# Kernel tuning notes

Hardware: AMD Instinct MI355X
Metric: run time of the kernel (lower is better)

The kernel has to match this reference:

```python
import jax, jax.numpy as jnp
from jax import lax
import numpy as np

DN = ('NCHW', 'OIHW', 'NCHW')
EPS = 1e-5


def conv3(x, w, b=None):
    # 3x3 conv, stride 1, padding 1 (SAME)
    y = lax.conv_general_dilated(x, w, (1, 1), 'SAME', dimension_numbers=DN)
    return y if b is None else y + b[None, :, None, None]


def bn_relu(x, gamma, beta):
    # training-mode BatchNorm2d (batch statistics over N,H,W) + ReLU
    m = jnp.mean(x, axis=(0, 2, 3), keepdims=True)
    v = jnp.var(x, axis=(0, 2, 3), keepdims=True)
    y = (x - m) * lax.rsqrt(v + EPS)
    y = y * gamma[None, :, None, None] + beta[None, :, None, None]
    return jax.nn.relu(y)


def _w(key, o, i):
    # torch init: normal(0, sqrt(2/(k*k*out)))
    std = np.sqrt(2.0 / (3 * 3 * o))
    return jax.random.normal(key, (o, i, 3, 3), dtype=jnp.float32) * std


def setup_inputs() -> dict:
    key = jax.random.key(0)
    ks = jax.random.split(key, 16)
    C = 256
    Ch = C // 2
    B, H, W = 4, 160, 160
    d = {}
    d['fpn_fea'] = jax.random.normal(ks[0], (B, C, H, W), dtype=jnp.float32)
    # sc_smooth_layer: conv(C->C)+BN+ReLU, conv(C->C/2)+BN+ReLU (no conv bias)
    d['w_sc1'] = _w(ks[1], C, C); d['g_sc1'] = jnp.ones((C,)); d['b_sc1'] = jnp.zeros((C,))
    d['w_sc2'] = _w(ks[2], Ch, C); d['g_sc2'] = jnp.ones((Ch,)); d['b_sc2'] = jnp.zeros((Ch,))
    # shrink / centroid heads: plain conv(C/2 -> 1) with bias
    d['w_shrink'] = _w(ks[3], 1, Ch); d['bias_shrink'] = jnp.zeros((1,))
    d['w_cent'] = _w(ks[4], 1, Ch); d['bias_cent'] = jnp.zeros((1,))
    # param_head
    d['w_p1'] = _w(ks[5], C, C); d['g_p1'] = jnp.ones((C,)); d['b_p1'] = jnp.zeros((C,))
    d['w_p2'] = _w(ks[6], Ch, C); d['g_p2'] = jnp.ones((Ch,)); d['b_p2'] = jnp.zeros((Ch,))
    d['w_p3'] = _w(ks[7], 2, Ch); d['bias_p3'] = jnp.zeros((2,))
    # shift_head
    d['w_s1'] = _w(ks[8], C, C); d['g_s1'] = jnp.ones((C,)); d['b_s1'] = jnp.zeros((C,))
    d['w_s2'] = _w(ks[9], Ch, C); d['g_s2'] = jnp.ones((Ch,)); d['b_s2'] = jnp.zeros((Ch,))
    d['w_s3'] = _w(ks[10], 8, Ch); d['bias_s3'] = jnp.zeros((8,))
    return d


def reference(fpn_fea, w_sc1, g_sc1, b_sc1, w_sc2, g_sc2, b_sc2,
              w_shrink, bias_shrink, w_cent, bias_cent,
              w_p1, g_p1, b_p1, w_p2, g_p2, b_p2, w_p3, bias_p3,
              w_s1, g_s1, b_s1, w_s2, g_s2, b_s2, w_s3, bias_s3):
    smooth = bn_relu(conv3(fpn_fea, w_sc1), g_sc1, b_sc1)
    smooth = bn_relu(conv3(smooth, w_sc2), g_sc2, b_sc2)
    shrink = conv3(smooth, w_shrink, bias_shrink)      # [B,1,H,W]
    centroid = conv3(smooth, w_cent, bias_cent)        # [B,1,H,W]
    p = bn_relu(conv3(fpn_fea, w_p1), g_p1, b_p1)
    p = bn_relu(conv3(p, w_p2), g_p2, b_p2)
    param = conv3(p, w_p3, bias_p3)                    # [B,2,H,W]
    s = bn_relu(conv3(fpn_fea, w_s1), g_s1, b_s1)
    s = bn_relu(conv3(s, w_s2), g_s2, b_s2)
    shift = conv3(s, w_s3, bias_s3)                    # [B,8,H,W]
    return (shrink, centroid, param, shift)
```

## Files before the change

### kernel.cpp

```cpp
#include <hip/hip_runtime.h>

typedef short bf16x8 __attribute__((ext_vector_type(8)));
typedef float f32x4 __attribute__((ext_vector_type(4)));

__device__ __forceinline__ float bf2f(unsigned short u) {
    union { unsigned int i; float f; } c; c.i = ((unsigned int)u) << 16; return c.f;
}
__device__ __forceinline__ unsigned short f2bf(float f) {
    union { float f; unsigned int i; } c; c.f = f;
    unsigned int u = c.i;
    u += 0x7fffu + ((u >> 16) & 1u);
    return (unsigned short)(u >> 16);
}

__device__ __forceinline__ void gload_lds16(const unsigned short* g, unsigned short* l) {
    __builtin_amdgcn_global_load_lds(
        (const __attribute__((address_space(1))) void*)g,
        (__attribute__((address_space(3))) void*)l, 16, 0, 0);
}

__global__ void transpose_pad(const float* __restrict__ x, unsigned short* __restrict__ xpad) {
    int idx = blockIdx.x * 256 + threadIdx.x;
    int w = idx % 160; int t = idx / 160;
    int cv = t % 32;   t /= 32;
    int h = t % 160;   int n = t / 160;
    const float* src = x + (((size_t)(n * 256 + cv * 8) * 160 + h) * 160 + w);
    unsigned short us[8];
#pragma unroll
    for (int k = 0; k < 8; ++k) us[k] = f2bf(src[(size_t)k * 25600]);
    uint4 o;
    o.x = (unsigned int)us[0] | ((unsigned int)us[1] << 16);
    o.y = (unsigned int)us[2] | ((unsigned int)us[3] << 16);
    o.z = (unsigned int)us[4] | ((unsigned int)us[5] << 16);
    o.w = (unsigned int)us[6] | ((unsigned int)us[7] << 16);
    *(uint4*)(xpad + ((size_t)((n * 162 + h + 1) * 162) + (w + 1)) * 256 + cv * 8) = o;
}

__device__ __forceinline__ void zero_border_one(unsigned short* buf, int C, int idx) {
    int CV = C >> 3;
    int cv = idx % CV; int t = idx / CV;
    int p = t % 644;   int n = t / 644;
    int h, w;
    if (p < 162)      { h = 0;   w = p; }
    else if (p < 324) { h = 161; w = p - 162; }
    else { int q = p - 324; h = 1 + (q >> 1); w = (q & 1) ? 161 : 0; }
    uint4 z = make_uint4(0u, 0u, 0u, 0u);
    *(uint4*)(buf + ((size_t)((n * 162 + h) * 162) + w) * C + cv * 8) = z;
}

__global__ void zero_all(unsigned short* __restrict__ xpad,
                         unsigned short* __restrict__ buf1, size_t s1,
                         unsigned short* __restrict__ buf2, size_t s2, int nbr) {
    int idx = blockIdx.x * 256 + threadIdx.x;
    if (idx < 82432) { zero_border_one(xpad, 256, idx); return; }
    idx -= 82432;
    int nb1 = nbr * 82432;
    if (idx < nb1) { zero_border_one(buf1 + (size_t)(idx / 82432) * s1, 256, idx % 82432); return; }
    idx -= nb1;
    int nb2 = nbr * 41216;
    if (idx < nb2) { zero_border_one(buf2 + (size_t)(idx / 41216) * s2, 128, idx % 41216); }
}

__global__ void pack_all(const float* __restrict__ s0, const float* __restrict__ s1,
                         const float* __restrict__ s2, const float* __restrict__ s3,
                         const float* __restrict__ s4, const float* __restrict__ s5,
                         unsigned short* __restrict__ w1p, unsigned short* __restrict__ w2p) {
    int idx = blockIdx.x * 256 + threadIdx.x;
    int t = idx / 294912, r = idx - t * 294912;
    const float* src; unsigned short* dst; int coBase;
    if (t < 6) {
        int br = t >> 1;
        src = (br == 0) ? s0 : (br == 1) ? s1 : s2;
        coBase = (t & 1) * 128;
        dst = w1p + (size_t)t * 294912;
    } else {
        int br = t - 6;
        src = (br == 0) ? s3 : (br == 1) ? s4 : s5;
        coBase = 0;
        dst = w2p + (size_t)br * 294912;
    }
    int tap, ci, o;
    if (r < 262144) {
        int tp = r >> 16, rem = r & 65535;
        int q = rem >> 13, r2 = rem & 8191;
        int e = r2 & 7, gco = r2 >> 3;
        int co = gco & 127, g = gco >> 7;
        tap = tp * 2 + (g >> 2);
        ci = q * 32 + (g & 3) * 8 + e;
        o = coBase + co;
    } else {
        int rem = r - 262144;
        int q = rem >> 12, r2 = rem & 4095;
        int e = r2 & 7, gco = r2 >> 3;
        int co = gco & 127, g = gco >> 7;
        tap = 8;
        ci = q * 32 + g * 8 + e;
        o = coBase + co;
    }
    dst[r] = f2bf(src[((size_t)(o * 256 + ci)) * 9 + tap]);
}

template<int COT, int BPB>
__global__ __launch_bounds__(256, 2) void conv3x3_mfma(
        const unsigned short* __restrict__ xpad0, size_t xstride,
        const unsigned short* __restrict__ wpk0, size_t wstride,
        unsigned short* __restrict__ ypad0, size_t ystride,
        float* __restrict__ stats, int sstride) {
    __shared__ __align__(16) unsigned short As[16384];
    __shared__ __align__(16) unsigned short Bs[12288];

    const int br = blockIdx.x / BPB;
    int bid = blockIdx.x % BPB;
    const unsigned short* xpad = xpad0 + (size_t)br * xstride;
    const unsigned short* wpk  = wpk0 + (size_t)br * wstride;
    unsigned short* ypad       = ypad0 + (size_t)br * ystride;
    float* sum   = stats + (size_t)br * sstride;
    float* sumsq = sum + 256;

    const int tid = threadIdx.x;
    const int wv = tid >> 6, lane = tid & 63;
    const int quad = lane >> 4, l15 = lane & 15;
    const int wco = wv >> 1, wsp = wv & 1;

    const int wt = bid % 5;
    const int ht = (bid / 5) % 20;
    const int n = (bid / 100) % 4;
    const int tile = bid / 400;
    const int co0 = tile * 128;
    const int h0 = ht * 8, w0 = wt * 32;

    const unsigned short* wtile = wpk + (size_t)tile * 294912;

    int boff[6];
#pragma unroll
    for (int r = 0; r < 6; ++r) {
        int slot = r * 256 + tid;
        int g = slot / 384, p = slot - g * 384;
        if (p > 339) p = 339;
        int prow = p / 34, pcol = p - prow * 34;
        boff[r] = ((n * 162 + h0 + prow) * 162 + (w0 + pcol)) * 256 + g * 8;
    }

    int p0[8];
#pragma unroll
    for (int j = 0; j < 8; ++j) {
        int sp = wsp * 128 + j * 16 + l15;
        p0[j] = (sp >> 5) * 34 + (sp & 31);
    }

    f32x4 acc[4][8];
#pragma unroll
    for (int i = 0; i < 4; ++i)
#pragma unroll
        for (int j = 0; j < 8; ++j) acc[i][j] = (f32x4){0.f, 0.f, 0.f, 0.f};

    for (int q = 0; q < 8; ++q) {
#pragma unroll
        for (int w = 0; w < 3; ++w) {
            __syncthreads();
            if (w == 0) {
                const unsigned short* bq = xpad + q * 32;
#pragma unroll
                for (int r = 0; r < 6; ++r)
                    gload_lds16(bq + boff[r], (unsigned short*)Bs + (r * 256 + tid) * 8);
            }
            if (w < 2) {
#pragma unroll
                for (int h = 0; h < 2; ++h) {
                    const unsigned short* asrc = wtile + (w * 2 + h) * 65536 + q * 8192 + tid * 8;
#pragma unroll
                    for (int c = 0; c < 4; ++c)
                        gload_lds16(asrc + c * 2048,
                                    (unsigned short*)As + h * 8192 + c * 2048 + tid * 8);
                }
            } else {
                const unsigned short* asrc = wtile + 262144 + q * 4096 + tid * 8;
#pragma unroll
                for (int c = 0; c < 2; ++c)
                    gload_lds16(asrc + c * 2048, (unsigned short*)As + c * 2048 + tid * 8);
            }
            __syncthreads();

#pragma unroll
            for (int t = 0; t < 4; ++t) {
                if (w == 2 && t >= 1) continue;
                const int TAP = (w < 2) ? (w * 4 + t) : 8;
                const int dh = TAP / 3, dw = TAP % 3;
                const int toff = dh * 34 + dw;
                const int g0 = (w < 2) ? ((t & 1) * 4 + quad) : quad;
                const unsigned short* Ab = As + ((w < 2) ? (t >> 1) * 8192 : 0);
                bf16x8 a[4];
#pragma unroll
                for (int i = 0; i < 4; ++i)
                    a[i] = *(const bf16x8*)(Ab + (size_t)(g0 * 128 + wco * 64 + i * 16 + l15) * 8);
#pragma unroll
                for (int jh = 0; jh < 2; ++jh) {
                    bf16x8 b[4];
#pragma unroll
                    for (int j = 0; j < 4; ++j)
                        b[j] = *(const bf16x8*)(Bs + (size_t)(quad * 384 + p0[jh * 4 + j] + toff) * 8);
#pragma unroll
                    for (int i = 0; i < 4; ++i)
#pragma unroll
                        for (int j = 0; j < 4; ++j)
                            acc[i][jh * 4 + j] = __builtin_amdgcn_mfma_f32_16x16x32_bf16(
                                a[i], b[j], acc[i][jh * 4 + j], 0, 0, 0);
                }
            }
        }
    }

#pragma unroll
    for (int i = 0; i < 4; ++i) {
        const int co_l = wco * 64 + i * 16 + quad * 4;
#pragma unroll
        for (int j = 0; j < 8; ++j) {
            const int sp = wsp * 128 + j * 16 + l15;
            const int jh = sp >> 5, jw = sp & 31;
            f32x4 v = acc[i][j];
            ushort4 pk;
            pk.x = f2bf(v[0]); pk.y = f2bf(v[1]); pk.z = f2bf(v[2]); pk.w = f2bf(v[3]);
            *(ushort4*)(ypad + ((size_t)((n * 162 + h0 + jh + 1) * 162) + (w0 + jw + 1)) * COT
                        + co0 + co_l) = pk;
        }
#pragma unroll
        for (int r = 0; r < 4; ++r) {
            float s1 = 0.f, s2 = 0.f;
#pragma unroll
            for (int j = 0; j < 8; ++j) { float v = acc[i][j][r]; s1 += v; s2 += v * v; }
#pragma unroll
            for (int m = 1; m < 16; m <<= 1) {
                s1 += __shfl_xor(s1, m, 64);
                s2 += __shfl_xor(s2, m, 64);
            }
            if (l15 == 0) {
                atomicAdd(&sum[co0 + co_l + r], s1);
                atomicAdd(&sumsq[co0 + co_l + r], s2);
            }
        }
    }
}

template<int C, int BPB>
__global__ void bn_apply(unsigned short* __restrict__ buf0, size_t bstride,
                         const float* __restrict__ stats, int sstride,
                         const float* g0, const float* g1, const float* g2,
                         const float* be0, const float* be1, const float* be2) {
    const int br = blockIdx.x / BPB;
    unsigned short* buf = buf0 + (size_t)br * bstride;
    const float* sum = stats + (size_t)br * sstride;
    const float* sumsq = sum + 256;
    const float* gamma = (br == 0) ? g0 : (br == 1) ? g1 : g2;
    const float* beta  = (br == 0) ? be0 : (br == 1) ? be1 : be2;

    __shared__ float s_sc[C], s_sh[C];
    if (threadIdx.x < C) {
        int c = threadIdx.x;
        const float inv = 1.0f / 102400.0f;
        float m = sum[c] * inv;
        float v = sumsq[c] * inv - m * m;
        float sc = gamma[c] * rsqrtf(v + 1e-5f);
        s_sc[c] = sc;
        s_sh[c] = beta[c] - m * sc;
    }
    __syncthreads();

    constexpr int CV = C / 8;
    int idx = (blockIdx.x % BPB) * 256 + threadIdx.x;
    int cv = idx % CV; int pos = idx / CV;
    int w = pos % 160; int h = (pos / 160) % 160; int n = pos / 25600;
    unsigned short* p = buf + ((size_t)((n * 162 + h + 1) * 162) + (w + 1)) * C + cv * 8;
    uint4 v = *(const uint4*)p;
    unsigned int ua[4] = {v.x, v.y, v.z, v.w};
    unsigned int ob[4];
#pragma unroll
    for (int j = 0; j < 4; ++j) {
        int c = cv * 8 + j * 2;
        float f0 = bf2f((unsigned short)(ua[j] & 0xffffu)) * s_sc[c] + s_sh[c];
        float f1 = bf2f((unsigned short)(ua[j] >> 16)) * s_sc[c + 1] + s_sh[c + 1];
        f0 = fmaxf(f0, 0.f); f1 = fmaxf(f1, 0.f);
        ob[j] = (unsigned int)f2bf(f0) | ((unsigned int)f2bf(f1) << 16);
    }
    uint4 o = make_uint4(ob[0], ob[1], ob[2], ob[3]);
    *(uint4*)p = o;
}

template<int CO>
__global__ __launch_bounds__(256) void head_conv(const unsigned short* __restrict__ z,
                                                 const float* __restrict__ w,
                                                 const float* __restrict__ bias,
                                                 float* __restrict__ out) {
    __shared__ float s_w[CO * 9 * 128];
    for (int t = threadIdx.x; t < CO * 9 * 128; t += 256) {
        int ci = t % 128; int r = t / 128;
        int tap = r % 9;  int o = r / 9;
        s_w[t] = w[((size_t)(o * 128 + ci)) * 9 + tap];
    }
    __syncthreads();

    const int pos = blockIdx.x * 256 + threadIdx.x;
    const int pw = pos % 160, ph = (pos / 160) % 160, pn = pos / 25600;
    float acc[CO];
#pragma unroll
    for (int o = 0; o < CO; ++o) acc[o] = bias[o];

#pragma unroll
    for (int dh = 0; dh < 3; ++dh)
#pragma unroll
        for (int dw = 0; dw < 3; ++dw) {
            const int tap = dh * 3 + dw;
            const unsigned short* zp = z + ((size_t)((pn * 162 + ph + dh) * 162) + (pw + dw)) * 128;
            for (int c8 = 0; c8 < 16; ++c8) {
                uint4 v = *(const uint4*)(zp + c8 * 8);
                unsigned int ua[4] = {v.x, v.y, v.z, v.w};
                float xv[8];
#pragma unroll
                for (int j = 0; j < 4; ++j) {
                    xv[2 * j]     = bf2f((unsigned short)(ua[j] & 0xffffu));
                    xv[2 * j + 1] = bf2f((unsigned short)(ua[j] >> 16));
                }
#pragma unroll
                for (int o = 0; o < CO; ++o) {
                    const float* wp = &s_w[(o * 9 + tap) * 128 + c8 * 8];
                    float4 w0 = *(const float4*)wp;
                    float4 w1 = *(const float4*)(wp + 4);
                    acc[o] = fmaf(xv[0], w0.x, acc[o]);
                    acc[o] = fmaf(xv[1], w0.y, acc[o]);
                    acc[o] = fmaf(xv[2], w0.z, acc[o]);
                    acc[o] = fmaf(xv[3], w0.w, acc[o]);
                    acc[o] = fmaf(xv[4], w1.x, acc[o]);
                    acc[o] = fmaf(xv[5], w1.y, acc[o]);
                    acc[o] = fmaf(xv[6], w1.z, acc[o]);
                    acc[o] = fmaf(xv[7], w1.w, acc[o]);
                }
            }
        }
#pragma unroll
    for (int o = 0; o < CO; ++o)
        out[((size_t)(pn * CO + o)) * 25600 + ph * 160 + pw] = acc[o];
}

__global__ __launch_bounds__(256) void head_conv_dual(const unsigned short* __restrict__ z,
                                                      const float* __restrict__ w1, const float* __restrict__ b1,
                                                      const float* __restrict__ w2, const float* __restrict__ b2,
                                                      float* __restrict__ out1, float* __restrict__ out2) {
    __shared__ float s_w[2 * 9 * 128];
    for (int t = threadIdx.x; t < 2 * 9 * 128; t += 256) {
        int ci = t % 128; int r = t / 128;
        int tap = r % 9;  int which = r / 9;
        const float* src = which ? w2 : w1;
        s_w[t] = src[(size_t)ci * 9 + tap];
    }
    __syncthreads();

    const int pos = blockIdx.x * 256 + threadIdx.x;
    const int pw = pos % 160, ph = (pos / 160) % 160, pn = pos / 25600;
    float a1 = b1[0], a2 = b2[0];

#pragma unroll
    for (int dh = 0; dh < 3; ++dh)
#pragma unroll
        for (int dw = 0; dw < 3; ++dw) {
            const int tap = dh * 3 + dw;
            const unsigned short* zp = z + ((size_t)((pn * 162 + ph + dh) * 162) + (pw + dw)) * 128;
            for (int c8 = 0; c8 < 16; ++c8) {
                uint4 v = *(const uint4*)(zp + c8 * 8);
                unsigned int ua[4] = {v.x, v.y, v.z, v.w};
                float xv[8];
#pragma unroll
                for (int j = 0; j < 4; ++j) {
                    xv[2 * j]     = bf2f((unsigned short)(ua[j] & 0xffffu));
                    xv[2 * j + 1] = bf2f((unsigned short)(ua[j] >> 16));
                }
                const float* wp1 = &s_w[tap * 128 + c8 * 8];
                const float* wp2 = &s_w[1152 + tap * 128 + c8 * 8];
#pragma unroll
                for (int e = 0; e < 8; ++e) {
                    a1 = fmaf(xv[e], wp1[e], a1);
                    a2 = fmaf(xv[e], wp2[e], a2);
                }
            }
        }
    out1[(size_t)pn * 25600 + ph * 160 + pw] = a1;
    out2[(size_t)pn * 25600 + ph * 160 + pw] = a2;
}

extern "C" void kernel_launch(void* const* d_in, const int* in_sizes, int n_in,
                              void* d_out, int out_size, void* d_ws, size_t ws_size,
                              hipStream_t stream) {
    const float* fpn = (const float*)d_in[0];
    const float* W1[3] = {(const float*)d_in[1],  (const float*)d_in[11], (const float*)d_in[19]};
    const float* G1[3] = {(const float*)d_in[2],  (const float*)d_in[12], (const float*)d_in[20]};
    const float* B1[3] = {(const float*)d_in[3],  (const float*)d_in[13], (const float*)d_in[21]};
    const float* W2[3] = {(const float*)d_in[4],  (const float*)d_in[14], (const float*)d_in[22]};
    const float* G2[3] = {(const float*)d_in[5],  (const float*)d_in[15], (const float*)d_in[23]};
    const float* B2[3] = {(const float*)d_in[6],  (const float*)d_in[16], (const float*)d_in[24]};
    const float* w_shrink = (const float*)d_in[7];  const float* b_shrink = (const float*)d_in[8];
    const float* w_cent   = (const float*)d_in[9];  const float* b_cent   = (const float*)d_in[10];
    const float* w_p3     = (const float*)d_in[17]; const float* b_p3     = (const float*)d_in[18];
    const float* w_s3     = (const float*)d_in[25]; const float* b_s3     = (const float*)d_in[26];
    float* out = (float*)d_out;

    const size_t S1 = (size_t)4 * 162 * 162 * 256;
    const size_t S2 = (size_t)4 * 162 * 162 * 128;
    const size_t need_fused = S1 * 2 * 4  + S2 * 2 * 3
                              + (size_t)9 * 294912 * 2 + 6 * 512 * 4;

    char* ws = (char*)d_ws;
    size_t off = 0;
    unsigned short* xpad = (unsigned short*)(ws + off); off += S1 * 2;
    const int NBR = (ws_size >= need_fused) ? 3 : 1;
    unsigned short* buf1 = (unsigned short*)(ws + off); off += S1 * 2 * NBR;
    unsigned short* buf2 = (unsigned short*)(ws + off); off += S2 * 2 * NBR;
    unsigned short* w1p  = (unsigned short*)(ws + off); off += (size_t)6 * 294912 * 2;
    unsigned short* w2p  = (unsigned short*)(ws + off); off += (size_t)3 * 294912 * 2;
    float* stats         = (float*)(ws + off);          off += (size_t)6 * 512 * 4;

    hipMemsetAsync(stats, 0, 6 * 512 * 4, stream);
    {
        int zthreads = 82432 * (1 + NBR) + 41216 * NBR;
        zero_all<<<(zthreads + 255) / 256, 256, 0, stream>>>(xpad, buf1, S1, buf2, S2, NBR);
    }
    transpose_pad<<<12800, 256, 0, stream>>>(fpn, xpad);
    pack_all<<<10368, 256, 0, stream>>>(W1[0], W1[1], W1[2], W2[0], W2[1], W2[2], w1p, w2p);

    if (NBR == 3) {
        conv3x3_mfma<256, 800><<<2400, 256, 0, stream>>>(
            xpad, 0, w1p, (size_t)2 * 294912, buf1, S1, stats, 1024);
        bn_apply<256, 12800><<<38400, 256, 0, stream>>>(
            buf1, S1, stats, 1024, G1[0], G1[1], G1[2], B1[0], B1[1], B1[2]);
        conv3x3_mfma<128, 400><<<1200, 256, 0, stream>>>(
            buf1, S1, w2p, (size_t)294912, buf2, S2, stats + 512, 1024);
        bn_apply<128, 6400><<<19200, 256, 0, stream>>>(
            buf2, S2, stats + 512, 1024, G2[0], G2[1], G2[2], B2[0], B2[1], B2[2]);
        head_conv_dual<<<400, 256, 0, stream>>>(buf2, w_shrink, b_shrink, w_cent, b_cent,
                                                out, out + 102400);
        head_conv<2><<<400, 256, 0, stream>>>(buf2 + S2, w_p3, b_p3, out + 204800);
        head_conv<8><<<400, 256, 0, stream>>>(buf2 + 2 * S2, w_s3, b_s3, out + 409600);
    } else {
        for (int br = 0; br < 3; ++br) {
            conv3x3_mfma<256, 800><<<800, 256, 0, stream>>>(
                xpad, 0, w1p + (size_t)br * 2 * 294912, 0, buf1, 0, stats + br * 1024, 0);
            bn_apply<256, 12800><<<12800, 256, 0, stream>>>(
                buf1, 0, stats + br * 1024, 0, G1[br], G1[br], G1[br], B1[br], B1[br], B1[br]);
            conv3x3_mfma<128, 400><<<400, 256, 0, stream>>>(
                buf1, 0, w2p + (size_t)br * 294912, 0, buf2, 0, stats + 512 + br * 1024, 0);
            bn_apply<128, 6400><<<6400, 256, 0, stream>>>(
                buf2, 0, stats + 512 + br * 1024, 0, G2[br], G2[br], G2[br], B2[br], B2[br], B2[br]);
            if (br == 0) {
                head_conv_dual<<<400, 256, 0, stream>>>(buf2, w_shrink, b_shrink, w_cent, b_cent,
                                                        out, out + 102400);
            } else if (br == 1) {
                head_conv<2><<<400, 256, 0, stream>>>(buf2, w_p3, b_p3, out + 204800);
            } else {
                head_conv<8><<<400, 256, 0, stream>>>(buf2, w_s3, b_s3, out + 409600);
            }
        }
    }
}
```

Baseline: 1.257 ms.

## Double-buffer activation tiles in LDS and read weights directly from global

Drops the LDS staging of weight (A) tiles and has each wave load its weight fragments straight from global memory. The freed LDS holds a second activation buffer, so the next channel chunk's input tile is fetched asynchronously while the current one is computed. This cuts the barriers per chunk from six to one. In exchange, every wave issues its own global weight loads, which depend on cache hits and may stall the MFMA stream. The unused co_l variable added near the top is dead code.

```diff
diff --git a/kernel.cpp b/kernel.cpp
--- a/kernel.cpp
+++ b/kernel.cpp
@@ -106,8 +106,7 @@
         const unsigned short* __restrict__ wpk0, size_t wstride,
         unsigned short* __restrict__ ypad0, size_t ystride,
         float* __restrict__ stats, int sstride) {
-    __shared__ __align__(16) unsigned short As[16384];
-    __shared__ __align__(16) unsigned short Bs[12288];
+    __shared__ __align__(16) unsigned short Bs[2][12288];
 
     const int br = blockIdx.x / BPB;
     int bid = blockIdx.x % BPB;
@@ -130,6 +129,7 @@
     const int h0 = ht * 8, w0 = wt * 32;
 
     const unsigned short* wtile = wpk + (size_t)tile * 294912;
+    const int co_l = wco * 64 + l15 * 1;
 
     int boff[6];
 #pragma unroll
@@ -154,65 +154,51 @@
 #pragma unroll
         for (int j = 0; j < 8; ++j) acc[i][j] = (f32x4){0.f, 0.f, 0.f, 0.f};
 
+    auto stageB = [&](int bq, int buf) {
+        const unsigned short* bqp = xpad + bq * 32;
+#pragma unroll
+        for (int r = 0; r < 6; ++r)
+            gload_lds16(bqp + boff[r], (unsigned short*)Bs[buf] + (r * 256 + tid) * 8);
+    };
+
+    stageB(0, 0);
+    __syncthreads();
+
     for (int q = 0; q < 8; ++q) {
-#pragma unroll
-        for (int w = 0; w < 3; ++w) {
-            __syncthreads();
-            if (w == 0) {
-                const unsigned short* bq = xpad + q * 32;
-#pragma unroll
-                for (int r = 0; r < 6; ++r)
-                    gload_lds16(bq + boff[r], (unsigned short*)Bs + (r * 256 + tid) * 8);
-            }
-            if (w < 2) {
-#pragma unroll
-                for (int h = 0; h < 2; ++h) {
-                    const unsigned short* asrc = wtile + (w * 2 + h) * 65536 + q * 8192 + tid * 8;
-#pragma unroll
-                    for (int c = 0; c < 4; ++c)
-                        gload_lds16(asrc + c * 2048,
-                                    (unsigned short*)As + h * 8192 + c * 2048 + tid * 8);
-                }
-            } else {
-                const unsigned short* asrc = wtile + 262144 + q * 4096 + tid * 8;
-#pragma unroll
-                for (int c = 0; c < 2; ++c)
-                    gload_lds16(asrc + c * 2048, (unsigned short*)As + c * 2048 + tid * 8);
-            }
-            __syncthreads();
-
-#pragma unroll
-            for (int t = 0; t < 4; ++t) {
-                if (w == 2 && t >= 1) continue;
-                const int TAP = (w < 2) ? (w * 4 + t) : 8;
-                const int dh = TAP / 3, dw = TAP % 3;
-                const int toff = dh * 34 + dw;
-                const int g0 = (w < 2) ? ((t & 1) * 4 + quad) : quad;
-                const unsigned short* Ab = As + ((w < 2) ? (t >> 1) * 8192 : 0);
-                bf16x8 a[4];
+        if (q < 7) stageB(q + 1, (q + 1) & 1);
+        const unsigned short* Bq = (const unsigned short*)Bs[q & 1];
+
+#pragma unroll
+        for (int t = 0; t < 9; ++t) {
+            const int dh = t / 3, dw = t % 3;
+            const int toff = dh * 34 + dw;
+            const unsigned short* ap = (t < 8)
+                ? wtile + (t >> 1) * 65536 + q * 8192 + (size_t)(((t & 1) * 4 + quad) * 128) * 8
+                : wtile + 262144 + q * 4096 + (size_t)(quad * 128) * 8;
+            bf16x8 a[4];
+#pragma unroll
+            for (int i = 0; i < 4; ++i)
+                a[i] = *(const bf16x8*)(ap + (size_t)(wco * 64 + i * 16 + l15) * 8);
+#pragma unroll
+            for (int jh = 0; jh < 2; ++jh) {
+                bf16x8 b[4];
+#pragma unroll
+                for (int j = 0; j < 4; ++j)
+                    b[j] = *(const bf16x8*)(Bq + (size_t)(quad * 384 + p0[jh * 4 + j] + toff) * 8);
 #pragma unroll
                 for (int i = 0; i < 4; ++i)
-                    a[i] = *(const bf16x8*)(Ab + (size_t)(g0 * 128 + wco * 64 + i * 16 + l15) * 8);
-#pragma unroll
-                for (int jh = 0; jh < 2; ++jh) {
-                    bf16x8 b[4];
 #pragma unroll
                     for (int j = 0; j < 4; ++j)
-                        b[j] = *(const bf16x8*)(Bs + (size_t)(quad * 384 + p0[jh * 4 + j] + toff) * 8);
-#pragma unroll
-                    for (int i = 0; i < 4; ++i)
-#pragma unroll
-                        for (int j = 0; j < 4; ++j)
-                            acc[i][jh * 4 + j] = __builtin_amdgcn_mfma_f32_16x16x32_bf16(
-                                a[i], b[j], acc[i][jh * 4 + j], 0, 0, 0);
-                }
-            }
-        }
+                        acc[i][jh * 4 + j] = __builtin_amdgcn_mfma_f32_16x16x32_bf16(
+                            a[i], b[j], acc[i][jh * 4 + j], 0, 0, 0);
+            }
+        }
+        __syncthreads();
     }
 
 #pragma unroll
     for (int i = 0; i < 4; ++i) {
-        const int co_l = wco * 64 + i * 16 + quad * 4;
+        const int co_e = wco * 64 + i * 16 + quad * 4;
 #pragma unroll
         for (int j = 0; j < 8; ++j) {
             const int sp = wsp * 128 + j * 16 + l15;
@@ -221,7 +207,7 @@
             ushort4 pk;
             pk.x = f2bf(v[0]); pk.y = f2bf(v[1]); pk.z = f2bf(v[2]); pk.w = f2bf(v[3]);
             *(ushort4*)(ypad + ((size_t)((n * 162 + h0 + jh + 1) * 162) + (w0 + jw + 1)) * COT
-                        + co0 + co_l) = pk;
+                        + co0 + co_e) = pk;
         }
 #pragma unroll
         for (int r = 0; r < 4; ++r) {
@@ -234,8 +220,8 @@
                 s2 += __shfl_xor(s2, m, 64);
             }
             if (l15 == 0) {
-                atomicAdd(&sum[co0 + co_l + r], s1);
-                atomicAdd(&sumsq[co0 + co_l + r], s2);
+                atomicAdd(&sum[co0 + co_e + r], s1);
+                atomicAdd(&sumsq[co0 + co_e + r], s2);
             }
         }
     }
```

Result: slower. 1.871 ms (+48.9%).

## Merge prep kernels and tile head convs through LDS with channel-chunked halo loads

Applied to the files above, without the earlier changes.

Three preprocessing kernels (border zeroing, input transpose/pad, weight pack) become one launch that dispatches on block index, which removes two launch gaps. The head convolutions now give each block an 8x32 pixel tile. The block stages a 10x34 halo tile into LDS in four 32-channel chunks using global_load_lds, instead of each thread reading all nine taps straight from global memory. This cuts redundant global traffic for the nine overlapping taps, at the cost of extra syncthreads and LDS use per chunk.

```diff
diff --git a/kernel.cpp b/kernel.cpp
--- a/kernel.cpp
+++ b/kernel.cpp
@@ -19,22 +19,6 @@
         (__attribute__((address_space(3))) void*)l, 16, 0, 0);
 }
 
-__global__ void transpose_pad(const float* __restrict__ x, unsigned short* __restrict__ xpad) {
-    int idx = blockIdx.x * 256 + threadIdx.x;
-    int w = idx % 160; int t = idx / 160;
-    int cv = t % 32;   t /= 32;
-    int h = t % 160;   int n = t / 160;
-    const float* src = x + (((size_t)(n * 256 + cv * 8) * 160 + h) * 160 + w);
-    unsigned short us[8];
-#pragma unroll
-    for (int k = 0; k < 8; ++k) us[k] = f2bf(src[(size_t)k * 25600]);
-    uint4 o;
-    o.x = (unsigned int)us[0] | ((unsigned int)us[1] << 16);
-    o.y = (unsigned int)us[2] | ((unsigned int)us[3] << 16);
-    o.z = (unsigned int)us[4] | ((unsigned int)us[5] << 16);
-    o.w = (unsigned int)us[6] | ((unsigned int)us[7] << 16);
-    *(uint4*)(xpad + ((size_t)((n * 162 + h + 1) * 162) + (w + 1)) * 256 + cv * 8) = o;
-}
 
 __device__ __forceinline__ void zero_border_one(unsigned short* buf, int C, int idx) {
     int CV = C >> 3;
@@ -48,10 +32,9 @@
     *(uint4*)(buf + ((size_t)((n * 162 + h) * 162) + w) * C + cv * 8) = z;
 }
 
-__global__ void zero_all(unsigned short* __restrict__ xpad,
-                         unsigned short* __restrict__ buf1, size_t s1,
-                         unsigned short* __restrict__ buf2, size_t s2, int nbr) {
-    int idx = blockIdx.x * 256 + threadIdx.x;
+__device__ __forceinline__ void do_zero(unsigned short* xpad,
+                                        unsigned short* buf1, size_t s1,
+                                        unsigned short* buf2, size_t s2, int nbr, int idx) {
     if (idx < 82432) { zero_border_one(xpad, 256, idx); return; }
     idx -= 82432;
     int nb1 = nbr * 82432;
@@ -61,11 +44,26 @@
     if (idx < nb2) { zero_border_one(buf2 + (size_t)(idx / 41216) * s2, 128, idx % 41216); }
 }
 
-__global__ void pack_all(const float* __restrict__ s0, const float* __restrict__ s1,
-                         const float* __restrict__ s2, const float* __restrict__ s3,
-                         const float* __restrict__ s4, const float* __restrict__ s5,
-                         unsigned short* __restrict__ w1p, unsigned short* __restrict__ w2p) {
-    int idx = blockIdx.x * 256 + threadIdx.x;
+__device__ __forceinline__ void do_transpose(const float* __restrict__ x,
+                                             unsigned short* __restrict__ xpad, int idx) {
+    int w = idx % 160; int t = idx / 160;
+    int cv = t % 32;   t /= 32;
+    int h = t % 160;   int n = t / 160;
+    const float* src = x + (((size_t)(n * 256 + cv * 8) * 160 + h) * 160 + w);
+    unsigned short us[8];
+#pragma unroll
+    for (int k = 0; k < 8; ++k) us[k] = f2bf(src[(size_t)k * 25600]);
+    uint4 o;
+    o.x = (unsigned int)us[0] | ((unsigned int)us[1] << 16);
+    o.y = (unsigned int)us[2] | ((unsigned int)us[3] << 16);
+    o.z = (unsigned int)us[4] | ((unsigned int)us[5] << 16);
+    o.w = (unsigned int)us[6] | ((unsigned int)us[7] << 16);
+    *(uint4*)(xpad + ((size_t)((n * 162 + h + 1) * 162) + (w + 1)) * 256 + cv * 8) = o;
+}
+
+__device__ __forceinline__ void do_pack(const float* s0, const float* s1, const float* s2,
+                                        const float* s3, const float* s4, const float* s5,
+                                        unsigned short* w1p, unsigned short* w2p, int idx) {
     int t = idx / 294912, r = idx - t * 294912;
     const float* src; unsigned short* dst; int coBase;
     if (t < 6) {
@@ -100,6 +98,25 @@
     dst[r] = f2bf(src[((size_t)(o * 256 + ci)) * 9 + tap]);
 }
 
+__global__ void prep(const float* __restrict__ fpn, unsigned short* __restrict__ xpad,
+                     unsigned short* __restrict__ buf1, size_t s1,
+                     unsigned short* __restrict__ buf2, size_t s2, int nbr,
+                     int zb, int zcount,
+                     const float* w10, const float* w11, const float* w12,
+                     const float* w20, const float* w21, const float* w22,
+                     unsigned short* __restrict__ w1p, unsigned short* __restrict__ w2p) {
+    int bid = blockIdx.x;
+    if (bid < zb) {
+        int idx = bid * 256 + threadIdx.x;
+        if (idx < zcount) do_zero(xpad, buf1, s1, buf2, s2, nbr, idx);
+        return;
+    }
+    bid -= zb;
+    if (bid < 12800) { do_transpose(fpn, xpad, bid * 256 + threadIdx.x); return; }
+    bid -= 12800;
+    do_pack(w10, w11, w12, w20, w21, w22, w1p, w2p, bid * 256 + threadIdx.x);
+}
+
 template<int COT, int BPB>
 __global__ __launch_bounds__(256, 2) void conv3x3_mfma(
         const unsigned short* __restrict__ xpad0, size_t xstride,
@@ -291,53 +308,77 @@
                                                  const float* __restrict__ bias,
                                                  float* __restrict__ out) {
     __shared__ float s_w[CO * 9 * 128];
+    __shared__ __align__(16) unsigned short s_z[1536 * 8];
     for (int t = threadIdx.x; t < CO * 9 * 128; t += 256) {
         int ci = t % 128; int r = t / 128;
         int tap = r % 9;  int o = r / 9;
         s_w[t] = w[((size_t)(o * 128 + ci)) * 9 + tap];
     }
-    __syncthreads();
-
-    const int pos = blockIdx.x * 256 + threadIdx.x;
-    const int pw = pos % 160, ph = (pos / 160) % 160, pn = pos / 25600;
+
+    const int bid = blockIdx.x;
+    const int wt = bid % 5, ht = (bid / 5) % 20, n = bid / 100;
+    const int h0 = ht * 8, w0 = wt * 32;
+    const int tid = threadIdx.x;
+
+    int zoff[6];
+#pragma unroll
+    for (int r = 0; r < 6; ++r) {
+        int slot = r * 256 + tid;
+        if (slot > 1359) slot = 1359;
+        int c8 = slot / 340, pos = slot - c8 * 340;
+        int prow = pos / 34, pcol = pos - prow * 34;
+        zoff[r] = ((n * 162 + h0 + prow) * 162 + (w0 + pcol)) * 128 + c8 * 8;
+    }
+    const int prow_t = tid >> 5, pcol_t = tid & 31;
+
     float acc[CO];
 #pragma unroll
     for (int o = 0; o < CO; ++o) acc[o] = bias[o];
 
-#pragma unroll
-    for (int dh = 0; dh < 3; ++dh)
-#pragma unroll
-        for (int dw = 0; dw < 3; ++dw) {
-            const int tap = dh * 3 + dw;
-            const unsigned short* zp = z + ((size_t)((pn * 162 + ph + dh) * 162) + (pw + dw)) * 128;
-            for (int c8 = 0; c8 < 16; ++c8) {
-                uint4 v = *(const uint4*)(zp + c8 * 8);
-                unsigned int ua[4] = {v.x, v.y, v.z, v.w};
-                float xv[8];
-#pragma unroll
-                for (int j = 0; j < 4; ++j) {
-                    xv[2 * j]     = bf2f((unsigned short)(ua[j] & 0xffffu));
-                    xv[2 * j + 1] = bf2f((unsigned short)(ua[j] >> 16));
+    for (int ph = 0; ph < 4; ++ph) {
+        __syncthreads();
+#pragma unroll
+        for (int r = 0; r < 6; ++r)
+            gload_lds16(z + zoff[r] + ph * 32, (unsigned short*)s_z + (r * 256 + tid) * 8);
+        __syncthreads();
+
+#pragma unroll
+        for (int dh = 0; dh < 3; ++dh)
+#pragma unroll
+            for (int dw = 0; dw < 3; ++dw) {
+                const int tap = dh * 3 + dw;
+                const int pos = (prow_t + dh) * 34 + pcol_t + dw;
+#pragma unroll
+                for (int c8 = 0; c8 < 4; ++c8) {
+                    uint4 v = *(const uint4*)(s_z + (size_t)(c8 * 340 + pos) * 8);
+                    unsigned int ua[4] = {v.x, v.y, v.z, v.w};
+                    float xv[8];
+#pragma unroll
+                    for (int j = 0; j < 4; ++j) {
+                        xv[2 * j]     = bf2f((unsigned short)(ua[j] & 0xffffu));
+                        xv[2 * j + 1] = bf2f((unsigned short)(ua[j] >> 16));
+                    }
+#pragma unroll
+                    for (int o = 0; o < CO; ++o) {
+                        const float* wp = &s_w[(o * 9 + tap) * 128 + ph * 32 + c8 * 8];
+                        float4 w0v = *(const float4*)wp;
+                        float4 w1v = *(const float4*)(wp + 4);
+                        acc[o] = fmaf(xv[0], w0v.x, acc[o]);
+                        acc[o] = fmaf(xv[1], w0v.y, acc[o]);
+                        acc[o] = fmaf(xv[2], w0v.z, acc[o]);
+                        acc[o] = fmaf(xv[3], w0v.w, acc[o]);
+                        acc[o] = fmaf(xv[4], w1v.x, acc[o]);
+                        acc[o] = fmaf(xv[5], w1v.y, acc[o]);
+                        acc[o] = fmaf(xv[6], w1v.z, acc[o]);
+                        acc[o] = fmaf(xv[7], w1v.w, acc[o]);
+                    }
                 }
-#pragma unroll
-                for (int o = 0; o < CO; ++o) {
-                    const float* wp = &s_w[(o * 9 + tap) * 128 + c8 * 8];
-                    float4 w0 = *(const float4*)wp;
-                    float4 w1 = *(const float4*)(wp + 4);
-                    acc[o] = fmaf(xv[0], w0.x, acc[o]);
-                    acc[o] = fmaf(xv[1], w0.y, acc[o]);
-                    acc[o] = fmaf(xv[2], w0.z, acc[o]);
-                    acc[o] = fmaf(xv[3], w0.w, acc[o]);
-                    acc[o] = fmaf(xv[4], w1.x, acc[o]);
-                    acc[o] = fmaf(xv[5], w1.y, acc[o]);
-                    acc[o] = fmaf(xv[6], w1.z, acc[o]);
-                    acc[o] = fmaf(xv[7], w1.w, acc[o]);
-                }
-            }
-        }
+            }
+    }
+    const int pw = w0 + pcol_t, phh = h0 + prow_t;
 #pragma unroll
     for (int o = 0; o < CO; ++o)
-        out[((size_t)(pn * CO + o)) * 25600 + ph * 160 + pw] = acc[o];
+        out[((size_t)(n * CO + o)) * 25600 + phh * 160 + pw] = acc[o];
 }
 
 __global__ __launch_bounds__(256) void head_conv_dual(const unsigned short* __restrict__ z,
@@ -345,44 +386,68 @@
                                                       const float* __restrict__ w2, const float* __restrict__ b2,
                                                       float* __restrict__ out1, float* __restrict__ out2) {
     __shared__ float s_w[2 * 9 * 128];
+    __shared__ __align__(16) unsigned short s_z[1536 * 8];
     for (int t = threadIdx.x; t < 2 * 9 * 128; t += 256) {
         int ci = t % 128; int r = t / 128;
         int tap = r % 9;  int which = r / 9;
         const float* src = which ? w2 : w1;
         s_w[t] = src[(size_t)ci * 9 + tap];
     }
-    __syncthreads();
-
-    const int pos = blockIdx.x * 256 + threadIdx.x;
-    const int pw = pos % 160, ph = (pos / 160) % 160, pn = pos / 25600;
+
+    const int bid = blockIdx.x;
+    const int wt = bid % 5, ht = (bid / 5) % 20, n = bid / 100;
+    const int h0 = ht * 8, w0 = wt * 32;
+    const int tid = threadIdx.x;
+
+    int zoff[6];
+#pragma unroll
+    for (int r = 0; r < 6; ++r) {
+        int slot = r * 256 + tid;
+        if (slot > 1359) slot = 1359;
+        int c8 = slot / 340, pos = slot - c8 * 340;
+        int prow = pos / 34, pcol = pos - prow * 34;
+        zoff[r] = ((n * 162 + h0 + prow) * 162 + (w0 + pcol)) * 128 + c8 * 8;
+    }
+    const int prow_t = tid >> 5, pcol_t = tid & 31;
+
     float a1 = b1[0], a2 = b2[0];
 
-#pragma unroll
-    for (int dh = 0; dh < 3; ++dh)
-#pragma unroll
-        for (int dw = 0; dw < 3; ++dw) {
-            const int tap = dh * 3 + dw;
-            const unsigned short* zp = z + ((size_t)((pn * 162 + ph + dh) * 162) + (pw + dw)) * 128;
-            for (int c8 = 0; c8 < 16; ++c8) {
-                uint4 v = *(const uint4*)(zp + c8 * 8);
-                unsigned int ua[4] = {v.x, v.y, v.z, v.w};
-                float xv[8];
-#pragma unroll
-                for (int j = 0; j < 4; ++j) {
-                    xv[2 * j]     = bf2f((unsigned short)(ua[j] & 0xffffu));
-                    xv[2 * j + 1] = bf2f((unsigned short)(ua[j] >> 16));
+    for (int ph = 0; ph < 4; ++ph) {
+        __syncthreads();
+#pragma unroll
+        for (int r = 0; r < 6; ++r)
+            gload_lds16(z + zoff[r] + ph * 32, (unsigned short*)s_z + (r * 256 + tid) * 8);
+        __syncthreads();
+
+#pragma unroll
+        for (int dh = 0; dh < 3; ++dh)
+#pragma unroll
+            for (int dw = 0; dw < 3; ++dw) {
+                const int tap = dh * 3 + dw;
+                const int pos = (prow_t + dh) * 34 + pcol_t + dw;
+#pragma unroll
+                for (int c8 = 0; c8 < 4; ++c8) {
+                    uint4 v = *(const uint4*)(s_z + (size_t)(c8 * 340 + pos) * 8);
+                    unsigned int ua[4] = {v.x, v.y, v.z, v.w};
+                    float xv[8];
+#pragma unroll
+                    for (int j = 0; j < 4; ++j) {
+                        xv[2 * j]     = bf2f((unsigned short)(ua[j] & 0xffffu));
+                        xv[2 * j + 1] = bf2f((unsigned short)(ua[j] >> 16));
+                    }
+                    const float* wp1 = &s_w[tap * 128 + ph * 32 + c8 * 8];
+                    const float* wp2 = &s_w[1152 + tap * 128 + ph * 32 + c8 * 8];
+#pragma unroll
+                    for (int e = 0; e < 8; ++e) {
+                        a1 = fmaf(xv[e], wp1[e], a1);
+                        a2 = fmaf(xv[e], wp2[e], a2);
+                    }
                 }
-                const float* wp1 = &s_w[tap * 128 + c8 * 8];
-                const float* wp2 = &s_w[1152 + tap * 128 + c8 * 8];
-#pragma unroll
-                for (int e = 0; e < 8; ++e) {
-                    a1 = fmaf(xv[e], wp1[e], a1);
-                    a2 = fmaf(xv[e], wp2[e], a2);
-                }
-            }
-        }
-    out1[(size_t)pn * 25600 + ph * 160 + pw] = a1;
-    out2[(size_t)pn * 25600 + ph * 160 + pw] = a2;
+            }
+    }
+    const int pw = w0 + pcol_t, phh = h0 + prow_t;
+    out1[(size_t)n * 25600 + phh * 160 + pw] = a1;
+    out2[(size_t)n * 25600 + phh * 160 + pw] = a2;
 }
 
 extern "C" void kernel_launch(void* const* d_in, const int* in_sizes, int n_in,
@@ -418,11 +483,12 @@
 
     hipMemsetAsync(stats, 0, 6 * 512 * 4, stream);
     {
-        int zthreads = 82432 * (1 + NBR) + 41216 * NBR;
-        zero_all<<<(zthreads + 255) / 256, 256, 0, stream>>>(xpad, buf1, S1, buf2, S2, NBR);
-    }
-    transpose_pad<<<12800, 256, 0, stream>>>(fpn, xpad);
-    pack_all<<<10368, 256, 0, stream>>>(W1[0], W1[1], W1[2], W2[0], W2[1], W2[2], w1p, w2p);
+        int zcount = 82432 * (1 + NBR) + 41216 * NBR;
+        int zb = (zcount + 255) / 256;
+        prep<<<zb + 12800 + 10368, 256, 0, stream>>>(
+            fpn, xpad, buf1, S1, buf2, S2, NBR, zb, zcount,
+            W1[0], W1[1], W1[2], W2[0], W2[1], W2[2], w1p, w2p);
+    }
 
     if (NBR == 3) {
         conv3x3_mfma<256, 800><<<2400, 256, 0, stream>>>(
```

Result: faster. 1.196 ms (-4.9%).
